# Kernel tuning notes

Hardware: AMD Instinct MI355X
Metric: run time of the kernel (lower is better)

Reference implementation:

```python
import jax, jax.numpy as jnp
import numpy as np

DIM = 64
HEADS = 16
HEAD_DIM = DIM // HEADS  # 4
CHUNK = 128
LN_EPS = 1e-5


def _ln(v, w, b):
    mu = jnp.mean(v, axis=-1, keepdims=True)
    var = jnp.var(v, axis=-1, keepdims=True)
    return (v - mu) * jax.lax.rsqrt(var + LN_EPS) * w + b


def setup_inputs() -> dict:
    key = jax.random.key(0)
    ks = jax.random.split(key, 16)
    B, C, H, W = 8, 64, 128, 128
    s = 0.02
    inp = {
        "x": jax.random.normal(ks[0], (B, C, H, W), jnp.float32),
        "text_embed": jax.random.normal(ks[1], (B, C, H, W), jnp.float32),
        # Linear weights stored as [in, out] (torch uses [out, in]; math identical via x @ W)
        "q_w": jax.random.normal(ks[2], (DIM, DIM), jnp.float32) * s,
        "q_b": jnp.zeros((DIM,), jnp.float32),
        "k_w": jax.random.normal(ks[3], (DIM, DIM), jnp.float32) * s,
        "k_b": jnp.zeros((DIM,), jnp.float32),
        "v_w": jax.random.normal(ks[4], (DIM, DIM), jnp.float32) * s,
        "v_b": jnp.zeros((DIM,), jnp.float32),
        "o_w": jax.random.normal(ks[5], (DIM, DIM), jnp.float32) * s,
        "o_b": jnp.zeros((DIM,), jnp.float32),
        "ln1_w": jnp.ones((DIM,), jnp.float32),
        "ln1_b": jnp.zeros((DIM,), jnp.float32),
        "ln2_w": jnp.ones((DIM,), jnp.float32),
        "ln2_b": jnp.zeros((DIM,), jnp.float32),
        "fc1_w": jax.random.normal(ks[6], (DIM, 4 * DIM), jnp.float32) * s,
        "fc1_b": jnp.zeros((4 * DIM,), jnp.float32),
        "fc2_w": jax.random.normal(ks[7], (4 * DIM, DIM), jnp.float32) * s,
        "fc2_b": jnp.zeros((DIM,), jnp.float32),
        # 1x1 conv as [out_ch, in_ch]
        "conv_w": jax.random.normal(ks[8], (DIM, DIM), jnp.float32) * s,
        "conv_b": jnp.zeros((DIM,), jnp.float32),
        # FiLM MLP: pooled_channels=64*4*4=1024 -> 128 -> 128
        "m1_w": jax.random.normal(ks[9], (1024, 2 * DIM), jnp.float32) * s,
        "m1_b": jnp.zeros((2 * DIM,), jnp.float32),
        "m2_w": jax.random.normal(ks[10], (2 * DIM, 2 * DIM), jnp.float32) * s,
        "m2_b": jnp.zeros((2 * DIM,), jnp.float32),
    }
    return inp


def reference(x, text_embed, q_w, q_b, k_w, k_b, v_w, v_b, o_w, o_b,
              ln1_w, ln1_b, ln2_w, ln2_b, fc1_w, fc1_b, fc2_w, fc2_b,
              conv_w, conv_b, m1_w, m1_b, m2_w, m2_b):
    B, C, H, W = x.shape
    N = H * W
    Nc = N // CHUNK  # number of local chunks (block-diagonal attention)
    scale = jnp.sqrt(jnp.float32(HEAD_DIM))

    prior_flat = text_embed.reshape(B, C, N).transpose(0, 2, 1)  # [B,N,C]
    x_flat = x.reshape(B, C, N).transpose(0, 2, 1)               # [B,N,C]

    prior_norm = _ln(prior_flat, ln1_w, ln1_b)
    Q = prior_norm @ q_w + q_b
    K = x_flat @ k_w + k_b
    V = x_flat @ v_w + v_b

    # blocked heads: [B, Nc, CHUNK, HEADS, HEAD_DIM]
    Qb = Q.reshape(B, Nc, CHUNK, HEADS, HEAD_DIM)
    Kb = K.reshape(B, Nc, CHUNK, HEADS, HEAD_DIM)
    Vb = V.reshape(B, Nc, CHUNK, HEADS, HEAD_DIM)

    scores = jnp.einsum('bnqhd,bnkhd->bnhqk', Qb, Kb) / scale  # [B,Nc,H,CHUNK,CHUNK]
    probs = jax.nn.softmax(scores, axis=-1)
    attn = jnp.einsum('bnhqk,bnkhd->bnqhd', probs, Vb).reshape(B, N, DIM)

    attn = attn @ o_w + o_b
    h = attn + prior_flat
    h_norm = _ln(h, ln2_w, ln2_b)
    ffn = jax.nn.gelu(h_norm @ fc1_w + fc1_b, approximate=False) @ fc2_w + fc2_b
    h = ffn + h

    h4 = h.transpose(0, 2, 1).reshape(B, DIM, H, W)
    conv = jnp.einsum('bihw,oi->bohw', h4, conv_w) + conv_b[None, :, None, None]
    out = conv + x  # TIAM output

    # FiLM: adaptive_avg_pool2d to (4,4) (H,W divisible by 4)
    te = text_embed.reshape(B, C, 4, H // 4, 4, W // 4).mean(axis=(3, 5))  # [B,C,4,4]
    te = te.reshape(B, -1)  # [B, 1024]
    hmlp = jax.nn.leaky_relu(te @ m1_w + m1_b, negative_slope=0.01)
    gb = hmlp @ m2_w + m2_b  # [B, 128]
    gamma = gb[:, :DIM][:, :, None, None]
    beta = gb[:, DIM:][:, :, None, None]
    return (1.0 + gamma) * out + beta
```

## Files before the change

### kernel.cpp

```cpp
#include <hip/hip_runtime.h>
#include <hip/hip_bf16.h>

#define NB 8
#define NTOK 16384
#define TOTTOK (NB*NTOK)

typedef __hip_bfloat16 bf16;
typedef __attribute__((ext_vector_type(8))) short bfrag;
typedef __attribute__((ext_vector_type(4))) float ffrag;

#define MFMA(a,b,c) __builtin_amdgcn_mfma_f32_16x16x32_bf16(a,b,c,0,0,0)

__device__ __forceinline__ float b2f(bf16 v){ return __bfloat162float(v); }
__device__ __forceinline__ bf16 f2b(float v){ return __float2bfloat16(v); }
__device__ __forceinline__ float bfu(unsigned short u){
    union { float f; unsigned v; } x; x.v = ((unsigned)u) << 16; return x.f; }
__device__ __forceinline__ unsigned short bu(bf16 b){
    union { bf16 b; unsigned short u; } x; x.b = b; return x.u; }
__device__ __forceinline__ void ld4(const bf16* p, float* f){
    uint2 r = *(const uint2*)p;
    f[0]=bfu(r.x & 0xffff); f[1]=bfu(r.x >> 16); f[2]=bfu(r.y & 0xffff); f[3]=bfu(r.y >> 16);
}
__device__ __forceinline__ float fastrcp(float x){
    float r; asm("v_rcp_f32 %0, %1" : "=v"(r) : "v"(x)); return r; }
__device__ __forceinline__ unsigned cvtpk(float lo, float hi){
    unsigned r; asm("v_cvt_pk_bf16_f32 %0,%1,%2" : "=v"(r) : "v"(lo), "v"(hi)); return r; }
__device__ __forceinline__ void stb(bf16* p, float v){
    unsigned r; asm("v_cvt_pk_bf16_f32 %0,%1,%1" : "=v"(r) : "v"(v));
    *(unsigned short*)p = (unsigned short)r; }
__device__ __forceinline__ float gelu_t(float x){
    float x2 = x*x;
    float y  = x * fmaf(x2, 0.1029425f, 2.3022077f);
    float z  = exp2f(y);
    float rc = fastrcp(z + 1.f);
    return x - x*rc;
}
__device__ __forceinline__ bfrag ld_frag(const bf16* p, int stride){
    int lane = threadIdx.x & 63;
    return *(const bfrag*)(p + (lane & 15)*stride + (lane >> 4)*8);
}

#define WI_QKV   0
#define WI_OW    13824
#define WI_CW    18432
#define WI_W1    23040
#define WI_W2    41472
#define WI_CONST 57856
#define WI_TOT   58752

__global__ __launch_bounds__(256) void wprep_kernel(
    const float* __restrict__ qw, const float* __restrict__ kw, const float* __restrict__ vw,
    const float* __restrict__ ow, const float* __restrict__ cw,
    const float* __restrict__ w1, const float* __restrict__ w2,
    const float* __restrict__ ln1w, const float* __restrict__ ln1b,
    const float* __restrict__ qb, const float* __restrict__ kb_, const float* __restrict__ vb,
    const float* __restrict__ ob, const float* __restrict__ ln2w, const float* __restrict__ ln2b,
    const float* __restrict__ b1, const float* __restrict__ b2, const float* __restrict__ cb,
    bf16* __restrict__ WI)
{
    int gid = blockIdx.x*256 + threadIdx.x;
    if (gid >= WI_TOT) return;
    float v = 0.f;
    if (gid < WI_OW){
        int m = gid / 4608, r = gid % 4608;
        int o = r / 72, ii = r % 72;
        const float* src = (m==0)? qw : (m==1)? kw : vw;
        if (ii < 64) v = src[ii*64 + o];
    } else if (gid < WI_CW){
        int r = gid - WI_OW;
        int o = r / 72, ii = r % 72;
        if (ii < 64) v = ow[ii*64 + o];
    } else if (gid < WI_W1){
        int r = gid - WI_CW;
        int co = r / 72, ii = r % 72;
        if (ii < 64) v = cw[co*64 + ii];
    } else if (gid < WI_W2){
        int r = gid - WI_W1;
        int gg = r / 2304, rr = r % 2304;
        int ol = rr / 72, ii = rr % 72;
        if (ii < 64) v = w1[ii*256 + gg*32 + ol];
    } else if (gid < WI_CONST){
        int a = gid - WI_W2;
        int o = a >> 8, ra = a & 255;
        int blk = ra >> 3, wi = ra & 7;
        int k = ((blk ^ (o & 7)) << 3) | wi;
        v = w2[k*64 + o];
    } else {
        int r = gid - WI_CONST;
        if      (r <  64) v = ln1w[r];
        else if (r < 128) v = ln1b[r-64];
        else if (r < 192) v = qb[r-128];
        else if (r < 256) v = kb_[r-192];
        else if (r < 320) v = vb[r-256];
        else if (r < 384) v = ob[r-320];
        else if (r < 448) v = ln2w[r-384];
        else if (r < 512) v = ln2b[r-448];
        else if (r < 768) v = b1[r-512];
        else if (r < 832) v = b2[r-768];
        else              v = cb[r-832];
    }
    WI[gid] = f2b(v);
}

__global__ __launch_bounds__(256) void transpose_kernel(
    const float* __restrict__ x, const float* __restrict__ te,
    bf16* __restrict__ xT, bf16* __restrict__ teT, float* __restrict__ pool)
{
    __shared__ bf16 T[64*66];
    int blk = blockIdx.x;
    int tile = blk & 255, b = blk >> 8;
    int t0 = tile * 64;
    const size_t sbase = (size_t)b*64*NTOK + t0;
    const size_t obase = ((size_t)b*NTOK + t0)*64;
    int tid = threadIdx.x;
    #pragma unroll
    for (int p = 0; p < 4; ++p){
        int c = p*16 + (tid >> 4), j4 = (tid & 15)*4;
        float4 v = *(const float4*)(x + sbase + (size_t)c*NTOK + j4);
        *(unsigned*)(T + c*66 + j4)     = cvtpk(v.x, v.y);
        *(unsigned*)(T + c*66 + j4 + 2) = cvtpk(v.z, v.w);
    }
    __syncthreads();
    #pragma unroll
    for (int p = 0; p < 4; ++p){
        int j = p*16 + (tid >> 4), c4 = (tid & 15)*4;
        uint2 o;
        o.x = (unsigned)bu(T[(c4+0)*66 + j]) | ((unsigned)bu(T[(c4+1)*66 + j]) << 16);
        o.y = (unsigned)bu(T[(c4+2)*66 + j]) | ((unsigned)bu(T[(c4+3)*66 + j]) << 16);
        *(uint2*)(xT + obase + (size_t)j*64 + c4) = o;
    }
    __syncthreads();
    #pragma unroll
    for (int p = 0; p < 4; ++p){
        int c = p*16 + (tid >> 4), j4 = (tid & 15)*4;
        float4 v = *(const float4*)(te + sbase + (size_t)c*NTOK + j4);
        *(unsigned*)(T + c*66 + j4)     = cvtpk(v.x, v.y);
        *(unsigned*)(T + c*66 + j4 + 2) = cvtpk(v.z, v.w);
    }
    __syncthreads();
    #pragma unroll
    for (int p = 0; p < 4; ++p){
        int j = p*16 + (tid >> 4), c4 = (tid & 15)*4;
        uint2 o;
        o.x = (unsigned)bu(T[(c4+0)*66 + j]) | ((unsigned)bu(T[(c4+1)*66 + j]) << 16);
        o.y = (unsigned)bu(T[(c4+2)*66 + j]) | ((unsigned)bu(T[(c4+3)*66 + j]) << 16);
        *(uint2*)(teT + obase + (size_t)j*64 + c4) = o;
    }
    if (tid < 128){
        int c = tid >> 1, hf = tid & 1;
        float s = 0.f;
        #pragma unroll
        for (int u = 0; u < 32; ++u) s += b2f(T[c*66 + hf*32 + u]);
        int h = t0 >> 7;
        int w0 = t0 & 127;
        int region = (h >> 5)*4 + ((w0 + hf*32) >> 5);
        atomicAdd(pool + b*1024 + c*16 + region, s);
    }
}

__global__ __launch_bounds__(128) void film_kernel(const float* __restrict__ pool,
        const float* __restrict__ m1w, const float* __restrict__ m1b,
        const float* __restrict__ m2w, const float* __restrict__ m2b,
        float* __restrict__ gb){
    int b = blockIdx.x; int j = threadIdx.x;
    __shared__ float tel[1024];
    __shared__ float hm[128];
    for (int i = j; i < 1024; i += 128) tel[i] = pool[b*1024 + i] * (1.f/1024.f);
    __syncthreads();
    float s = m1b[j];
    for (int i = 0; i < 1024; ++i) s = fmaf(tel[i], m1w[i*128 + j], s);
    hm[j] = (s > 0.f) ? s : 0.01f*s;
    __syncthreads();
    float g = m2b[j];
    for (int i = 0; i < 128; ++i) g = fmaf(hm[i], m2w[i*128 + j], g);
    gb[b*128 + j] = g;
}

#define OFF_TE2 0
#define OFF_XT  16384
#define OFF_PN  34816
#define OFF_WT  53248
#define OFF_W2T 47616
#define OFF_CON 80896
#define SCALE_Q 0.72134752044448170f

__device__ __forceinline__ void ln_phase(const bf16* S, bf16* D,
                                         const bf16* Wt, const bf16* Bs, int tid)
{
    int tok = tid >> 2, q4 = tid & 3;
    float vals[16];
    int op2[2];
    float s = 0.f, s2 = 0.f;
    #pragma unroll
    for (int u8 = 0; u8 < 2; ++u8){
        int o = (q4*2 + u8) ^ (tok & 7);
        op2[u8] = o;
        uint4 v = *(const uint4*)(S + tok*64 + o*8);
        const unsigned* ap = &v.x;
        float* vp = vals + u8*8;
        #pragma unroll
        for (int e = 0; e < 4; ++e){
            float lo = bfu(ap[e] & 0xffff), hi = bfu(ap[e] >> 16);
            vp[e*2] = lo; vp[e*2+1] = hi;
            s += lo + hi;
            s2 = fmaf(lo, lo, fmaf(hi, hi, s2));
        }
    }
    s  += __shfl_xor(s, 1, 64);  s2 += __shfl_xor(s2, 1, 64);
    s  += __shfl_xor(s, 2, 64);  s2 += __shfl_xor(s2, 2, 64);
    float mean = s * (1.f/64.f);
    float var  = s2 * (1.f/64.f) - mean*mean;
    float rstd = rsqrtf(var + 1e-5f);
    #pragma unroll
    for (int u8 = 0; u8 < 2; ++u8){
        int cc0 = op2[u8]*8;
        uint4 wv = *(const uint4*)(Wt + cc0);
        uint4 bv = *(const uint4*)(Bs + cc0);
        const unsigned* wp = &wv.x;
        const unsigned* bp = &bv.x;
        uint4 o; unsigned* opp = &o.x;
        #pragma unroll
        for (int e = 0; e < 4; ++e){
            float lo = (vals[u8*8+e*2]  -mean)*rstd*bfu(wp[e] & 0xffff) + bfu(bp[e] & 0xffff);
            float hi = (vals[u8*8+e*2+1]-mean)*rstd*bfu(wp[e] >> 16)    + bfu(bp[e] >> 16);
            opp[e] = cvtpk(lo, hi);
        }
        *(uint4*)(D + tok*72 + cc0) = o;
    }
}

__global__ __launch_bounds__(512,4) void mega_kernel(
    const bf16* __restrict__ xT, const bf16* __restrict__ teT, const float* __restrict__ x,
    const bf16* __restrict__ WI, const float* __restrict__ gb, float* __restrict__ out)
{
    __shared__ __align__(16) char sm[81920];
    bf16* TE2 = (bf16*)(sm + OFF_TE2);
    bf16* XT  = (bf16*)(sm + OFF_XT);
    bf16* PN  = (bf16*)(sm + OFF_PN);
    bf16* WT  = (bf16*)(sm + OFF_WT);
    bf16* VT  = (bf16*)(sm + OFF_WT);
    bf16* OWT = (bf16*)(sm + OFF_WT);
    bf16* W1S = (bf16*)(sm + OFF_PN);
    bf16* P   = (bf16*)(sm + OFF_PN + 4608);
    bf16* CWs = (bf16*)(sm + OFF_PN);
    bf16* W2T = (bf16*)(sm + OFF_W2T);
    bf16* CON = (bf16*)(sm + OFF_CON);
    bf16* OT  = (bf16*)(sm + OFF_TE2);

    int tid = threadIdx.x;
    int w = tid >> 6, lane = tid & 63;
    int g = lane >> 4, c = lane & 15;
    int t0g = blockIdx.x * 128;
    int b = t0g >> 14, n0 = t0g & (NTOK-1);
    const ffrag fz = {0.f,0.f,0.f,0.f};

    {
        const uint4* gx = (const uint4*)(xT + (size_t)t0g*64);
        const uint4* gt = (const uint4*)(teT + (size_t)t0g*64);
        #pragma unroll
        for (int p = 0; p < 2; ++p){
            int i = tid + p*512;
            int tok = i >> 3, seg = i & 7;
            *(uint4*)(XT + tok*72 + seg*8) = gx[i];
            ((uint4*)TE2)[i] = gt[i];
        }
        const uint4* wq = (const uint4*)(WI + WI_QKV);
        for (int i = tid; i < 1728; i += 512) ((uint4*)WT)[i] = wq[i];
        if (tid < 16) ((uint4*)CON)[tid] = ((const uint4*)(WI + WI_CONST))[tid];
    }
    __syncthreads();
    ln_phase(TE2, PN, CON, CON + 64, tid);
    __syncthreads();
    {
        if (tid < 24) ((uint4*)CON)[tid] = ((const uint4*)(WI + WI_CONST + 128))[tid];
        ffrag accQ[4], accK[4], accV[4];
        #pragma unroll
        for (int nt=0;nt<4;++nt){ accQ[nt]=fz; accK[nt]=fz; accV[nt]=fz; }
        bfrag aQ[2], aX[2];
        #pragma unroll
        for (int k2=0;k2<2;++k2){
            aQ[k2] = ld_frag(PN + (w*16)*72 + k2*32, 72);
            aX[k2] = ld_frag(XT + (w*16)*72 + k2*32, 72);
        }
        for (int nt = 0; nt < 4; ++nt){
            #pragma unroll
            for (int k2 = 0; k2 < 2; ++k2){
                bfrag bq2 = ld_frag(WT +        nt*16*72 + k2*32, 72);
                bfrag bk2 = ld_frag(WT + 4608 + nt*16*72 + k2*32, 72);
                bfrag bv2 = ld_frag(WT + 9216 + nt*16*72 + k2*32, 72);
                accQ[nt] = MFMA(aQ[k2], bq2, accQ[nt]);
                accK[nt] = MFMA(aX[k2], bk2, accK[nt]);
                accV[nt] = MFMA(aX[k2], bv2, accV[nt]);
            }
        }
        __syncthreads();
        int rq = g*4;
        #pragma unroll
        for (int nt=0;nt<4;++nt){
            int n = nt*16 + c;
            float bq3 = b2f(CON[n]), bk3 = b2f(CON[64+n]), bv3 = b2f(CON[128+n]);
            #pragma unroll
            for (int r=0;r<4;++r){
                int m = w*16 + rq + r;
                stb(PN + m*72 + n, (accQ[nt][r] + bq3) * SCALE_Q);
                stb(XT + m*72 + n, accK[nt][r] + bk3);
                int kp = ((m >> 6) << 6) + (m & 15)*4 + ((m >> 4) & 3);
                stb(VT + (5*(n>>2) + (n&3))*136 + kp, accV[nt][r] + bv3);
            }
        }
        if (tid < 256){
            int row = 5*(tid >> 4) + 4, col8 = (tid & 15)*8;
            uint4 ov; ov.x = ov.y = ov.z = ov.w = 0x3f803f80u;
            *(uint4*)(VT + row*136 + col8) = ov;
        }
    }
    __syncthreads();
    {
        bfrag bq[8];
        #pragma unroll
        for (int nt = 0; nt < 8; ++nt) bq[nt] = ld_frag(XT + nt*16*72 + (w>>2)*32, 72);
        __syncthreads();
        bf16* Pw = XT + w*1024;
        #pragma unroll 1
        for (int hh = 0; hh < 2; ++hh){
            int h = w*2 + hh;
            int ag = w & 3;
            bfrag bv4[4];
            #pragma unroll
            for (int kk = 0; kk < 4; ++kk)
                bv4[kk] = ld_frag(VT + (5*h)*136 + (kk>>1)*64 + (kk&1)*32, 136);
            #pragma unroll 2
            for (int qt = 0; qt < 8; ++qt){
                int q = qt*16 + c;
                uint2 qv = *(const uint2*)(PN + q*72 + h*4);
                union { bfrag f; uint2 u[2]; } A;
                uint2 z2; z2.x = 0u; z2.y = 0u;
                uint2 sel = (g == ag) ? qv : z2;
                if (hh){ A.u[0] = z2;  A.u[1] = sel; }
                else   { A.u[0] = sel; A.u[1] = z2;  }
                ffrag og = fz;
                #pragma unroll
                for (int kh = 0; kh < 2; ++kh){
                    ffrag acc[4];
                    #pragma unroll
                    for (int nt = 0; nt < 4; ++nt) acc[nt] = MFMA(A.f, bq[kh*4+nt], fz);
                    #pragma unroll
                    for (int nt = 0; nt < 4; ++nt){
                        #pragma unroll
                        for (int r = 0; r < 4; ++r) acc[nt][r] = exp2f(acc[nt][r]);
                    }
                    #pragma unroll
                    for (int r = 0; r < 4; ++r){
                        uint2 pk;
                        pk.x = cvtpk(acc[0][r], acc[1][r]);
                        pk.y = cvtpk(acc[2][r], acc[3][r]);
                        int row = 4*g + r;
                        *(uint2*)(Pw + row*64 + (((c>>1) ^ (row&7)) << 3) + ((c&1) << 2)) = pk;
                    }
                    #pragma unroll
                    for (int ks = 0; ks < 2; ++ks){
                        bfrag ap = *(const bfrag*)(Pw + c*64 + (((ks*4 + g) ^ (c&7)) << 3));
                        og = MFMA(ap, bv4[kh*2 + ks], og);
                    }
                }
                #pragma unroll
                for (int r = 0; r < 4; ++r){
                    float lr = __shfl(og[r], (lane & 48) | 4, 64);
                    if (c < 4)
                        stb(PN + (qt*16 + 4*g + r)*72 + h*4 + c, og[r] * fastrcp(lr));
                }
            }
        }
    }
    __syncthreads();
    {
        const uint4* oi = (const uint4*)(WI + WI_OW);
        for (int i = tid; i < 576; i += 512) ((uint4*)OWT)[i] = oi[i];
        if (tid < 24) ((uint4*)CON)[tid] = ((const uint4*)(WI + WI_CONST + 320))[tid];
        __syncthreads();
        ffrag acc2[4];
        #pragma unroll
        for (int nt=0;nt<4;++nt) acc2[nt] = fz;
        bfrag af2[2];
        #pragma unroll
        for (int k2=0;k2<2;++k2)
            af2[k2] = ld_frag(PN + (w*16)*72 + k2*32, 72);
        #pragma unroll
        for (int nt=0;nt<4;++nt){
            #pragma unroll
            for (int k2=0;k2<2;++k2){
                bfrag bf_ = ld_frag(OWT + nt*16*72 + k2*32, 72);
                acc2[nt] = MFMA(af2[k2], bf_, acc2[nt]);
            }
        }
        __syncthreads();
        int rq = g*4;
        #pragma unroll
        for (int nt=0;nt<4;++nt){
            int n = nt*16 + c;
            float bo = b2f(CON[n]);
            #pragma unroll
            for (int r=0;r<4;++r){
                int m = w*16 + rq + r;
                stb(XT + m*72 + n, acc2[nt][r] + bo);
            }
        }
    }
    __syncthreads();
    for (int j = tid; j < 1024; j += 512){
        int tok = j >> 3, c8 = (j & 7)*8;
        uint4 a = *(const uint4*)(TE2 + tok*64 + c8);
        uint4 bq2 = *(const uint4*)(XT + tok*72 + c8);
        const unsigned* ap = &a.x; const unsigned* bp = &bq2.x;
        uint4 o; unsigned* opp = &o.x;
        #pragma unroll
        for (int e = 0; e < 4; ++e){
            float lo = bfu(ap[e] & 0xffff) + bfu(bp[e] & 0xffff);
            float hi = bfu(ap[e] >> 16)    + bfu(bp[e] >> 16);
            opp[e] = cvtpk(lo, hi);
        }
        *(uint4*)(TE2 + tok*64 + c8) = o;
    }
    __syncthreads();
    ln_phase(TE2, XT, CON + 64, CON + 128, tid);
    __syncthreads();
    {
        const uint4* w2i = (const uint4*)(WI + WI_W2);
        for (int i = tid; i < 2048; i += 512) ((uint4*)W2T)[i] = w2i[i];
        if (tid < 48) ((uint4*)CON)[tid] = ((const uint4*)(WI + WI_CONST + 512))[tid];
        bfrag af[2];
        #pragma unroll
        for (int k2=0;k2<2;++k2)
            af[k2] = ld_frag(XT + (w*16)*72 + k2*32, 72);
        ffrag acc2[4];
        #pragma unroll
        for (int nt=0;nt<4;++nt) acc2[nt] = fz;
        int rq = g*4;
        const uint4* w1i = (const uint4*)(WI + WI_W1);
        uint4 pA;
        if (tid < 288) pA = w1i[tid];
        for (int gg = 0; gg < 8; ++gg){
            __syncthreads();
            if (tid < 288){
                ((uint4*)W1S)[tid] = pA;
                if (gg < 7) pA = w1i[(gg+1)*288 + tid];
            }
            __syncthreads();
            ffrag accg[2];
            #pragma unroll
            for (int ntl=0;ntl<2;++ntl) accg[ntl] = fz;
            #pragma unroll
            for (int ntl=0;ntl<2;++ntl){
                #pragma unroll
                for (int k2=0;k2<2;++k2){
                    bfrag bf_ = ld_frag(W1S + ntl*16*72 + k2*32, 72);
                    accg[ntl] = MFMA(af[k2], bf_, accg[ntl]);
                }
            }
            #pragma unroll
            for (int ntl=0;ntl<2;++ntl){
                int n = ntl*16 + c;
                float bb = b2f(CON[gg*32 + n]);
                #pragma unroll
                for (int r=0;r<4;++r){
                    int m = w*16 + rq + r;
                    float xv = accg[ntl][r] + bb;
                    stb(P + m*32 + ((((n>>3) ^ ((m>>1)&3)) << 3) | (n & 7)), gelu_t(xv));
                }
            }
            {
                int rr = w*16 + c;
                bfrag ap = *(const bfrag*)(P + rr*32 + ((g ^ ((rr>>1)&3)) << 3));
                #pragma unroll
                for (int nt=0;nt<4;++nt){
                    int n = nt*16 + c;
                    int chunk = gg*4 + g;
                    bfrag bf2 = *(const bfrag*)(W2T + n*256 + ((chunk ^ (n&7)) << 3));
                    acc2[nt] = MFMA(ap, bf2, acc2[nt]);
                }
            }
        }
        #pragma unroll
        for (int nt=0;nt<4;++nt){
            int n = nt*16 + c;
            float bb = b2f(CON[256+n]);
            #pragma unroll
            for (int r=0;r<4;++r){
                int m = w*16 + rq + r;
                stb(XT + m*72 + n, acc2[nt][r] + bb + b2f(TE2[m*64 + n]));
            }
        }
    }
    __syncthreads();
    {
        const uint4* ci = (const uint4*)(WI + WI_CW);
        for (int i = tid; i < 576; i += 512) ((uint4*)CWs)[i] = ci[i];
        __syncthreads();
        bfrag ac[2];
        #pragma unroll
        for (int k2=0;k2<2;++k2) ac[k2] = ld_frag(CWs + ((w&3)*16)*72 + k2*32, 72);
        int rq = g*4;
        #pragma unroll
        for (int nt4 = 0; nt4 < 4; ++nt4){
            int nt = (w>>2)*4 + nt4;
            ffrag accc = fz;
            #pragma unroll
            for (int k2=0;k2<2;++k2){
                bfrag bh = ld_frag(XT + nt*16*72 + k2*32, 72);
                accc = MFMA(ac[k2], bh, accc);
            }
            int tok = nt*16 + c;
            #pragma unroll
            for (int r=0;r<4;++r){
                int co = (w&3)*16 + rq + r;
                stb(OT + co*128 + tok, accc[r] + b2f(CON[320+co]));
            }
        }
    }
    __syncthreads();
    {
        int cc = tid >> 3, seg = (tid & 7)*16;
        float gamma = 1.f + gb[b*128 + cc];
        float beta  = gb[b*128 + 64 + cc];
        const size_t gbase = (size_t)b*64*NTOK + (size_t)cc*NTOK + n0 + seg;
        #pragma unroll
        for (int u = 0; u < 4; ++u){
            float cv[4];
            ld4(OT + cc*128 + seg + u*4, cv);
            float4 xv = *(const float4*)(x + gbase + u*4);
            float4 ov;
            ov.x = fmaf(gamma, cv[0]+xv.x, beta);
            ov.y = fmaf(gamma, cv[1]+xv.y, beta);
            ov.z = fmaf(gamma, cv[2]+xv.z, beta);
            ov.w = fmaf(gamma, cv[3]+xv.w, beta);
            *(float4*)(out + gbase + u*4) = ov;
        }
    }
}

extern "C" void kernel_launch(void* const* d_in, const int* in_sizes, int n_in,
                              void* d_out, int out_size, void* d_ws, size_t ws_size,
                              hipStream_t stream){
    const float* x   = (const float*)d_in[0];
    const float* te  = (const float*)d_in[1];
    const float* qw  = (const float*)d_in[2];
    const float* qb  = (const float*)d_in[3];
    const float* kw  = (const float*)d_in[4];
    const float* kb  = (const float*)d_in[5];
    const float* vw  = (const float*)d_in[6];
    const float* vb  = (const float*)d_in[7];
    const float* ow  = (const float*)d_in[8];
    const float* ob  = (const float*)d_in[9];
    const float* ln1w= (const float*)d_in[10];
    const float* ln1b= (const float*)d_in[11];
    const float* ln2w= (const float*)d_in[12];
    const float* ln2b= (const float*)d_in[13];
    const float* w1  = (const float*)d_in[14];
    const float* b1  = (const float*)d_in[15];
    const float* w2  = (const float*)d_in[16];
    const float* b2  = (const float*)d_in[17];
    const float* cw  = (const float*)d_in[18];
    const float* cb  = (const float*)d_in[19];
    const float* m1w = (const float*)d_in[20];
    const float* m1b = (const float*)d_in[21];
    const float* m2w = (const float*)d_in[22];
    const float* m2b = (const float*)d_in[23];

    char* ws = (char*)d_ws;
    const size_t BUF = (size_t)TOTTOK*64*2;
    bf16* xT  = (bf16*)(ws);
    bf16* teT = (bf16*)(ws + BUF);
    float* pool = (float*)(ws + 2*BUF);
    float* gbp  = (float*)(ws + 2*BUF + 32768);
    bf16* WI    = (bf16*)(ws + 2*BUF + 36864);

    hipMemsetAsync(pool, 0, 8*1024*sizeof(float), stream);
    wprep_kernel<<<(WI_TOT + 255)/256, 256, 0, stream>>>(
        qw, kw, vw, ow, cw, w1, w2,
        ln1w, ln1b, qb, kb, vb, ob, ln2w, ln2b, b1, b2, cb, WI);
    transpose_kernel<<<2048, 256, 0, stream>>>(x, te, xT, teT, pool);
    film_kernel<<<8, 128, 0, stream>>>(pool, m1w, m1b, m2w, m2b, gbp);
    mega_kernel<<<TOTTOK/128, 512, 0, stream>>>(xT, teT, x, WI, gbp, (float*)d_out);
}
```

Baseline: 309.0 us.

## Fuse input transpose into mega kernel and split pooling into dedicated kernel

```diff
diff --git a/kernel.cpp b/kernel.cpp
--- a/kernel.cpp
+++ b/kernel.cpp
@@ -102,60 +102,26 @@
     WI[gid] = f2b(v);
 }
 
-__global__ __launch_bounds__(256) void transpose_kernel(
-    const float* __restrict__ x, const float* __restrict__ te,
-    bf16* __restrict__ xT, bf16* __restrict__ teT, float* __restrict__ pool)
+__global__ __launch_bounds__(256) void pool_kernel(const float* __restrict__ te,
+                                                   float* __restrict__ pool)
 {
-    __shared__ bf16 T[64*66];
     int blk = blockIdx.x;
-    int tile = blk & 255, b = blk >> 8;
-    int t0 = tile * 64;
-    const size_t sbase = (size_t)b*64*NTOK + t0;
-    const size_t obase = ((size_t)b*NTOK + t0)*64;
+    const float* src = te + (size_t)blk * NTOK;
     int tid = threadIdx.x;
+    __shared__ float R[16];
+    if (tid < 16) R[tid] = 0.f;
+    __syncthreads();
+    int rw = (tid >> 3) & 3;
+    float acc[4] = {0.f, 0.f, 0.f, 0.f};
     #pragma unroll
-    for (int p = 0; p < 4; ++p){
-        int c = p*16 + (tid >> 4), j4 = (tid & 15)*4;
-        float4 v = *(const float4*)(x + sbase + (size_t)c*NTOK + j4);
-        *(unsigned*)(T + c*66 + j4)     = cvtpk(v.x, v.y);
-        *(unsigned*)(T + c*66 + j4 + 2) = cvtpk(v.z, v.w);
-    }
-    __syncthreads();
+    for (int u = 0; u < 16; ++u){
+        float4 v = *(const float4*)(src + u*1024 + tid*4);
+        acc[u >> 2] += v.x + v.y + v.z + v.w;
+    }
     #pragma unroll
-    for (int p = 0; p < 4; ++p){
-        int j = p*16 + (tid >> 4), c4 = (tid & 15)*4;
-        uint2 o;
-        o.x = (unsigned)bu(T[(c4+0)*66 + j]) | ((unsigned)bu(T[(c4+1)*66 + j]) << 16);
-        o.y = (unsigned)bu(T[(c4+2)*66 + j]) | ((unsigned)bu(T[(c4+3)*66 + j]) << 16);
-        *(uint2*)(xT + obase + (size_t)j*64 + c4) = o;
-    }
-    __syncthreads();
-    #pragma unroll
-    for (int p = 0; p < 4; ++p){
-        int c = p*16 + (tid >> 4), j4 = (tid & 15)*4;
-        float4 v = *(const float4*)(te + sbase + (size_t)c*NTOK + j4);
-        *(unsigned*)(T + c*66 + j4)     = cvtpk(v.x, v.y);
-        *(unsigned*)(T + c*66 + j4 + 2) = cvtpk(v.z, v.w);
-    }
-    __syncthreads();
-    #pragma unroll
-    for (int p = 0; p < 4; ++p){
-        int j = p*16 + (tid >> 4), c4 = (tid & 15)*4;
-        uint2 o;
-        o.x = (unsigned)bu(T[(c4+0)*66 + j]) | ((unsigned)bu(T[(c4+1)*66 + j]) << 16);
-        o.y = (unsigned)bu(T[(c4+2)*66 + j]) | ((unsigned)bu(T[(c4+3)*66 + j]) << 16);
-        *(uint2*)(teT + obase + (size_t)j*64 + c4) = o;
-    }
-    if (tid < 128){
-        int c = tid >> 1, hf = tid & 1;
-        float s = 0.f;
-        #pragma unroll
-        for (int u = 0; u < 32; ++u) s += b2f(T[c*66 + hf*32 + u]);
-        int h = t0 >> 7;
-        int w0 = t0 & 127;
-        int region = (h >> 5)*4 + ((w0 + hf*32) >> 5);
-        atomicAdd(pool + b*1024 + c*16 + region, s);
-    }
+    for (int rh = 0; rh < 4; ++rh) atomicAdd(&R[rh*4 + rw], acc[rh]);
+    __syncthreads();
+    if (tid < 16) pool[blk*16 + tid] = R[tid];
 }
 
 __global__ __launch_bounds__(128) void film_kernel(const float* __restrict__ pool,
@@ -230,7 +196,7 @@
 }
 
 __global__ __launch_bounds__(512,4) void mega_kernel(
-    const bf16* __restrict__ xT, const bf16* __restrict__ teT, const float* __restrict__ x,
+    const float* __restrict__ x, const float* __restrict__ te,
     const bf16* __restrict__ WI, const float* __restrict__ gb, float* __restrict__ out)
 {
     __shared__ __align__(16) char sm[81920];
@@ -255,21 +221,59 @@
     const ffrag fz = {0.f,0.f,0.f,0.f};
 
     {
-        const uint4* gx = (const uint4*)(xT + (size_t)t0g*64);
-        const uint4* gt = (const uint4*)(teT + (size_t)t0g*64);
+        bf16* Tx = PN;
+        bf16* Tt = WT;
+        if (tid < 16) ((uint4*)CON)[tid] = ((const uint4*)(WI + WI_CONST))[tid];
+        int c0 = tid >> 3, j16 = (tid & 7) * 16;
+        const float* xp = x  + (size_t)b*64*NTOK + (size_t)c0*NTOK + n0 + j16;
+        const float* tp = te + (size_t)b*64*NTOK + (size_t)c0*NTOK + n0 + j16;
+        float4 a0 = *(const float4*)(xp);
+        float4 a1 = *(const float4*)(xp + 4);
+        float4 a2 = *(const float4*)(xp + 8);
+        float4 a3 = *(const float4*)(xp + 12);
+        float4 e0 = *(const float4*)(tp);
+        float4 e1 = *(const float4*)(tp + 4);
+        float4 e2 = *(const float4*)(tp + 8);
+        float4 e3 = *(const float4*)(tp + 12);
+        uint4 o0, o1;
+        o0.x = cvtpk(a0.x, a0.y); o0.y = cvtpk(a0.z, a0.w);
+        o0.z = cvtpk(a1.x, a1.y); o0.w = cvtpk(a1.z, a1.w);
+        o1.x = cvtpk(a2.x, a2.y); o1.y = cvtpk(a2.z, a2.w);
+        o1.z = cvtpk(a3.x, a3.y); o1.w = cvtpk(a3.z, a3.w);
+        *(uint4*)(Tx + c0*136 + j16)     = o0;
+        *(uint4*)(Tx + c0*136 + j16 + 8) = o1;
+        o0.x = cvtpk(e0.x, e0.y); o0.y = cvtpk(e0.z, e0.w);
+        o0.z = cvtpk(e1.x, e1.y); o0.w = cvtpk(e1.z, e1.w);
+        o1.x = cvtpk(e2.x, e2.y); o1.y = cvtpk(e2.z, e2.w);
+        o1.z = cvtpk(e3.x, e3.y); o1.w = cvtpk(e3.z, e3.w);
+        *(uint4*)(Tt + c0*136 + j16)     = o0;
+        *(uint4*)(Tt + c0*136 + j16 + 8) = o1;
+        __syncthreads();
         #pragma unroll
         for (int p = 0; p < 2; ++p){
-            int i = tid + p*512;
-            int tok = i >> 3, seg = i & 7;
-            *(uint4*)(XT + tok*72 + seg*8) = gx[i];
-            ((uint4*)TE2)[i] = gt[i];
-        }
+            int idx = p*512 + tid;
+            int tok = idx & 127, seg = idx >> 7;
+            const bf16* rx = Tx + seg*1088 + tok;
+            const bf16* rt = Tt + seg*1088 + tok;
+            uint4 ox, ot;
+            ox.x = (unsigned)bu(rx[0])   | ((unsigned)bu(rx[136]) << 16);
+            ox.y = (unsigned)bu(rx[272]) | ((unsigned)bu(rx[408]) << 16);
+            ox.z = (unsigned)bu(rx[544]) | ((unsigned)bu(rx[680]) << 16);
+            ox.w = (unsigned)bu(rx[816]) | ((unsigned)bu(rx[952]) << 16);
+            *(uint4*)(XT + tok*72 + seg*8) = ox;
+            ot.x = (unsigned)bu(rt[0])   | ((unsigned)bu(rt[136]) << 16);
+            ot.y = (unsigned)bu(rt[272]) | ((unsigned)bu(rt[408]) << 16);
+            ot.z = (unsigned)bu(rt[544]) | ((unsigned)bu(rt[680]) << 16);
+            ot.w = (unsigned)bu(rt[952-136]) | ((unsigned)bu(rt[952]) << 16);
+            *(uint4*)(TE2 + tok*64 + seg*8) = ot;
+        }
+    }
+    __syncthreads();
+    {
+        ln_phase(TE2, PN, CON, CON + 64, tid);
         const uint4* wq = (const uint4*)(WI + WI_QKV);
         for (int i = tid; i < 1728; i += 512) ((uint4*)WT)[i] = wq[i];
-        if (tid < 16) ((uint4*)CON)[tid] = ((const uint4*)(WI + WI_CONST))[tid];
-    }
-    __syncthreads();
-    ln_phase(TE2, PN, CON, CON + 64, tid);
+    }
     __syncthreads();
     {
         if (tid < 24) ((uint4*)CON)[tid] = ((const uint4*)(WI + WI_CONST + 128))[tid];
@@ -393,7 +397,6 @@
                 acc2[nt] = MFMA(af2[k2], bf_, acc2[nt]);
             }
         }
-        __syncthreads();
         int rq = g*4;
         #pragma unroll
         for (int nt=0;nt<4;++nt){
@@ -402,24 +405,9 @@
             #pragma unroll
             for (int r=0;r<4;++r){
                 int m = w*16 + rq + r;
-                stb(XT + m*72 + n, acc2[nt][r] + bo);
-            }
-        }
-    }
-    __syncthreads();
-    for (int j = tid; j < 1024; j += 512){
-        int tok = j >> 3, c8 = (j & 7)*8;
-        uint4 a = *(const uint4*)(TE2 + tok*64 + c8);
-        uint4 bq2 = *(const uint4*)(XT + tok*72 + c8);
-        const unsigned* ap = &a.x; const unsigned* bp = &bq2.x;
-        uint4 o; unsigned* opp = &o.x;
-        #pragma unroll
-        for (int e = 0; e < 4; ++e){
-            float lo = bfu(ap[e] & 0xffff) + bfu(bp[e] & 0xffff);
-            float hi = bfu(ap[e] >> 16)    + bfu(bp[e] >> 16);
-            opp[e] = cvtpk(lo, hi);
-        }
-        *(uint4*)(TE2 + tok*64 + c8) = o;
+                stb(TE2 + m*64 + n, acc2[nt][r] + bo + b2f(TE2[m*64 + n]));
+            }
+        }
     }
     __syncthreads();
     ln_phase(TE2, XT, CON + 64, CON + 128, tid);
@@ -567,18 +555,14 @@
     const float* m2b = (const float*)d_in[23];
 
     char* ws = (char*)d_ws;
-    const size_t BUF = (size_t)TOTTOK*64*2;
-    bf16* xT  = (bf16*)(ws);
-    bf16* teT = (bf16*)(ws + BUF);
-    float* pool = (float*)(ws + 2*BUF);
-    float* gbp  = (float*)(ws + 2*BUF + 32768);
-    bf16* WI    = (bf16*)(ws + 2*BUF + 36864);
-
-    hipMemsetAsync(pool, 0, 8*1024*sizeof(float), stream);
+    float* pool = (float*)(ws);
+    float* gbp  = (float*)(ws + 32768);
+    bf16* WI    = (bf16*)(ws + 36864);
+
     wprep_kernel<<<(WI_TOT + 255)/256, 256, 0, stream>>>(
         qw, kw, vw, ow, cw, w1, w2,
         ln1w, ln1b, qb, kb, vb, ob, ln2w, ln2b, b1, b2, cb, WI);
-    transpose_kernel<<<2048, 256, 0, stream>>>(x, te, xT, teT, pool);
-    film_kernel<<<8, 128, 0, stream>>>(pool, m1w, m1b, m2w, m2b, gbp);
-    mega_kernel<<<TOTTOK/128, 512, 0, stream>>>(xT, teT, x, WI, gbp, (float*)d_out);
-}
+    pool_kernel<<<NB*64, 256, 0, stream>>>(te, pool);
+    film_kernel<<<NB, 128, 0, stream>>>(pool, m1w, m1b, m2w, m2b, gbp);
+    mega_kernel<<<TOTTOK/128, 512, 0, stream>>>(x, te, WI, gbp, (float*)d_out);
+}
```

Measured after the change: 285.8 us. 7.5% less time.
